# Optimization experiments

Hardware: AMD Instinct MI355X
Metric: run time of the kernel (lower is better)

Reference implementation:

```python
import jax, jax.numpy as jnp
import numpy as np

C = 1.0
SQC = C ** 0.5
EPS = 1e-15

def _artanh(x):
    return jnp.arctanh(jnp.clip(x, -1 + 1e-5, 1 - 1e-5))

def _norm(x):
    return jnp.sqrt(jnp.maximum(jnp.sum(x * x, -1, keepdims=True), EPS))

def expmap0(u):
    un = _norm(u)
    return jnp.tanh(SQC * un) * u / (SQC * un)

def logmap0(x):
    xn = _norm(x)
    return _artanh(SQC * xn) * x / (SQC * xn)

def project(x):
    maxnorm = (1.0 - 1e-3) / SQC
    xn = _norm(x)
    return jnp.where(xn > maxnorm, x / xn * maxnorm, x)

def mobius_add(x, y):
    x2 = jnp.sum(x * x, -1, keepdims=True)
    y2 = jnp.sum(y * y, -1, keepdims=True)
    xy = jnp.sum(x * y, -1, keepdims=True)
    num = (1 + 2 * C * xy + C * y2) * x + (1 - C * x2) * y
    den = 1 + 2 * C * xy + C * C * x2 * y2
    return num / jnp.maximum(den, EPS)

def mobius_matvec(M, x):
    xn = _norm(x)
    Mx = x @ M.T
    Mxn = _norm(Mx)
    res = jnp.tanh(Mxn / xn * _artanh(SQC * xn)) * Mx / (Mxn * SQC)
    return jnp.where(Mxn <= 1e-7, jnp.zeros_like(res), res)

def mobius_pointwise_mul(w, x):
    xn = _norm(x)
    wx = w * x
    wxn = _norm(wx)
    res = jnp.tanh(wxn / xn * _artanh(SQC * xn)) * wx / (wxn * SQC)
    return jnp.where(wxn <= 1e-7, jnp.zeros_like(res), res)

def mobius_scalar_mul(r, x):
    # r: [B,1] scalars, x: [P] point -> [B,P]
    xn = _norm(x)
    return jnp.tanh(r * _artanh(SQC * xn)) * x / (xn * SQC)

def poincare_dist(x, y):
    return 2.0 / SQC * _artanh(SQC * _norm(mobius_add(-x, y)))

def dist2plane(x, p, a):
    # x: [B,P], p,a: [K,P] -> [B,K]
    diff = mobius_add(-p[None, :, :], x[:, None, :])  # [B,K,P]
    diff2 = jnp.sum(diff * diff, -1)
    sc_da = jnp.sum(diff * a[None, :, :], -1)
    a_norm = jnp.sqrt(jnp.maximum(jnp.sum(a * a, -1), EPS))  # [K]
    num = 2 * SQC * sc_da
    den = jnp.maximum((1 - C * diff2) * a_norm[None, :], EPS)
    return jnp.arcsinh(num / den) / SQC

def one_rnn_transform(W, h, U, x, b):
    Wh = mobius_matvec(W, h)
    Ux = mobius_matvec(U, x)
    return mobius_add(mobius_add(Wh, Ux), b)

def mobius_gru(x_seq, w_ih, w_hh, b, h0):
    # x_seq: [S,B,E]; w_ih: [3,H,E]; w_hh: [3,H,H]; b: [3,H]
    W_ir, W_ih_, W_iz = w_ih[0], w_ih[1], w_ih[2]
    W_hr, W_hh_, W_hz = w_hh[0], w_hh[1], w_hh[2]
    b_r, b_h, b_z = b[0], b[1], b[2]

    def cell(h, x):
        z = jax.nn.sigmoid(logmap0(one_rnn_transform(W_hz, h, W_iz, x, b_z)))
        r = jax.nn.sigmoid(logmap0(one_rnn_transform(W_hr, h, W_ir, x, b_r)))
        rh = mobius_pointwise_mul(r, h)
        h_tilde = one_rnn_transform(W_hh_, rh, W_ih_, x, b_h)
        delta = mobius_add(-h, h_tilde)
        h_new = mobius_add(h, mobius_pointwise_mul(z, delta))
        return h_new, None

    h_final, _ = jax.lax.scan(cell, h0, x_seq)
    return h_final

def mobius_linear(x, W, b):
    return project(mobius_add(mobius_matvec(W, x), b))


def setup_inputs() -> dict:
    key = jax.random.key(0)
    ks = jax.random.split(key, 20)
    V, E, H, P, K, B, S = 32000, 256, 512, 256, 2, 512, 100
    inp = {
        "embedding": jax.random.normal(ks[0], (V, E), jnp.float32) * 0.1,
        "w_ih_src": jax.random.normal(ks[1], (3, H, E), jnp.float32) * 0.05,
        "w_hh_src": jax.random.normal(ks[2], (3, H, H), jnp.float32) * 0.05,
        "b_src": jax.random.normal(ks[3], (3, H), jnp.float32) * 0.01,
        "w_ih_tgt": jax.random.normal(ks[4], (3, H, E), jnp.float32) * 0.05,
        "w_hh_tgt": jax.random.normal(ks[5], (3, H, H), jnp.float32) * 0.05,
        "b_tgt": jax.random.normal(ks[6], (3, H), jnp.float32) * 0.01,
        "wp_src": jax.random.normal(ks[7], (P, H), jnp.float32) * 0.05,
        "bp_src": jax.random.normal(ks[8], (P,), jnp.float32) * 0.01,
        "wp_tgt": jax.random.normal(ks[9], (P, H), jnp.float32) * 0.05,
        "bp_tgt": jax.random.normal(ks[10], (P,), jnp.float32) * 0.01,
        "dist_bias": jax.random.normal(ks[11], (P,), jnp.float32) * 0.01,
        "plane_p": jax.random.normal(ks[12], (K, P), jnp.float32) * 0.01,
        "plane_a": jax.random.normal(ks[13], (K, P), jnp.float32) * 0.1,
        "source_tokens": jax.random.randint(ks[14], (B, S), 0, V, jnp.int32),
        "target_tokens": jax.random.randint(ks[15], (B, S), 0, V, jnp.int32),
        "alignment": jax.random.randint(ks[16], (B,), 0, B, jnp.int32),
    }
    return inp


def reference(embedding, w_ih_src, w_hh_src, b_src, w_ih_tgt, w_hh_tgt, b_tgt,
              wp_src, bp_src, wp_tgt, bp_tgt, dist_bias, plane_p, plane_a,
              source_tokens, target_tokens, alignment):
    B, S = source_tokens.shape
    H = w_hh_src.shape[-1]
    # euclidean embeddings lifted to the Poincare ball (embedding_type='eucl', hyp cell)
    src = expmap0(embedding[source_tokens]).transpose(1, 0, 2)  # [S,B,E]
    tgt = expmap0(embedding[target_tokens]).transpose(1, 0, 2)
    h0 = jnp.zeros((B, H), src.dtype)
    h_src = mobius_gru(src, w_ih_src, w_hh_src, b_src, h0)
    h_tgt = mobius_gru(tgt, w_ih_tgt, w_hh_tgt, b_tgt, h0)
    h_tgt = h_tgt[alignment]
    src_proj = mobius_linear(h_src, wp_src, bp_src)
    tgt_proj = mobius_linear(h_tgt, wp_tgt, bp_tgt)
    projected = mobius_add(src_proj, tgt_proj)
    d2 = poincare_dist(h_src, h_tgt) ** 2  # [B,1]
    bias = mobius_scalar_mul(d2, dist_bias)  # [B,P]
    projected = mobius_add(projected, bias)
    logits = dist2plane(projected, plane_p, plane_a)  # [B,K]
    return logits
```

## Files before the change

### kernel.cpp

```cpp
#include <hip/hip_runtime.h>
#include <hip/hip_bf16.h>

#define EPSF 1e-15f

__device__ __forceinline__ float artanh_c(float x) {
  x = fminf(fmaxf(x, -1.f + 1e-5f), 1.f - 1e-5f);
  return 0.5f * log1pf(2.f * x / (1.f - x));
}
__device__ __forceinline__ float sigmoidf(float x) {
  return 1.f / (1.f + expf(-x));
}

template<int N>
__device__ __forceinline__ void block_reduce(float* v) {
  __shared__ float s[4][N];
  __syncthreads();
  const int lane = threadIdx.x & 63;
  const int wv = threadIdx.x >> 6;
#pragma unroll
  for (int n = 0; n < N; n++) {
    float x = v[n];
#pragma unroll
    for (int o = 32; o > 0; o >>= 1) x += __shfl_down(x, o);
    if (lane == 0) s[wv][n] = x;
  }
  __syncthreads();
#pragma unroll
  for (int n = 0; n < N; n++) v[n] = s[0][n] + s[1][n] + s[2][n] + s[3][n];
}

__global__ __launch_bounds__(256) void k_tok(
    const float* __restrict__ emb, const int* __restrict__ src_t,
    const int* __restrict__ tgt_t, float4* __restrict__ tokf)
{
  const int item = blockIdx.x * 4 + (threadIdx.x >> 6);
  const int lane = threadIdx.x & 63;
  const int g = item / 51200;
  const int rem = item - g * 51200;
  const int b = rem / 100, s = rem - b * 100;
  const int tok = (g ? tgt_t : src_t)[b * 100 + s];
  const float4 v = ((const float4*)(emb + (size_t)tok * 256))[lane];
  float ss = v.x*v.x + v.y*v.y + v.z*v.z + v.w*v.w;
#pragma unroll
  for (int o = 32; o > 0; o >>= 1) ss += __shfl_xor(ss, o);
  if (lane == 0) {
    const float un = sqrtf(fmaxf(ss, EPSF));
    const float fac = tanhf(un) / un;
    const float xn = sqrtf(fmaxf(fac * fac * ss, EPSF));
    const float axn = artanh_c(xn);
    tokf[item] = make_float4(fac, xn, axn, un);
  }
}

__global__ __launch_bounds__(256) void kx0(
    const float* __restrict__ emb, const int* __restrict__ src_t,
    const int* __restrict__ tgt_t, const float4* __restrict__ tokf,
    float* __restrict__ xb)
{
  const int row = blockIdx.x;
  const int t = threadIdx.x;
  const int g = row >> 9, b = row & 511;
  const int tok = (g ? tgt_t : src_t)[b * 100];
  const float fac = tokf[(g * 512 + b) * 100].x;
  xb[(size_t)row * 256 + t] = fac * emb[(size_t)tok * 256 + t];
}

__global__ __launch_bounds__(256) void gemm_k(
    int mode,
    const float* __restrict__ hbuf, const float* __restrict__ xbuf,
    const float* __restrict__ rhbuf,
    const float* __restrict__ w_ih_src, const float* __restrict__ w_hh_src,
    const float* __restrict__ w_ih_tgt, const float* __restrict__ w_hh_tgt,
    const float* __restrict__ wp_src, const float* __restrict__ wp_tgt,
    const int* __restrict__ alignment,
    float* __restrict__ out)
{
  const int rt = blockIdx.x, ct = blockIdx.y;
  const int rowBase = rt * 64;
  const int tid = threadIdx.x;
  int kdim, ldo, colBase;
  const float* W;
  const float* Abase;
  int gather = 0;
  if (mode == 0) {
    const int chunk = ct >> 3;
    colBase = ct * 64; ldo = 2560;
    const int g = rowBase >> 9;
    const float* wih = g ? w_ih_tgt : w_ih_src;
    const float* whh = g ? w_hh_tgt : w_hh_src;
    if (chunk == 0)      { W = whh + 2 * 512 * 512; Abase = hbuf; kdim = 512; }
    else if (chunk == 1) { W = whh;                 Abase = hbuf; kdim = 512; }
    else {
      kdim = 256; Abase = xbuf;
      W = (chunk == 2) ? (wih + 2 * 512 * 256) : ((chunk == 3) ? wih : (wih + 512 * 256));
    }
    W += (size_t)((ct & 7) * 64) * kdim;
  } else if (mode == 1) {
    const int g = rowBase >> 9;
    W = (g ? w_hh_tgt : w_hh_src) + 512 * 512 + (size_t)(ct * 64) * 512;
    Abase = rhbuf; kdim = 512; ldo = 512; colBase = ct * 64;
  } else {
    const int chunk = ct >> 2;
    colBase = ct * 64; ldo = 512; kdim = 512;
    W = (chunk ? wp_tgt : wp_src) + (size_t)((ct & 3) * 64) * 512;
    Abase = hbuf;
    gather = chunk;
  }
  const int ar = tid >> 2, ak = (tid & 3) * 4;
  int arow = rowBase + ar;
  if (mode == 2 && gather) arow = 512 + alignment[arow];
  const float* Arow = Abase + (size_t)arow * kdim;
  const float* Wrow = W + (size_t)(tid >> 2) * kdim + (tid & 3) * 4;

  __shared__ __align__(16) float As[16][68];
  __shared__ __align__(16) float Bs[16][68];
  float acc[4][4] = {{0.f}};
  const int ty = tid >> 4, tx = tid & 15;

  for (int k0 = 0; k0 < kdim; k0 += 16) {
    const float4 av = *(const float4*)(Arow + k0 + ak);
    const float4 bv = *(const float4*)(Wrow + k0);
    const int bj = tid >> 2;
    As[ak + 0][ar] = av.x; As[ak + 1][ar] = av.y; As[ak + 2][ar] = av.z; As[ak + 3][ar] = av.w;
    Bs[ak + 0][bj] = bv.x; Bs[ak + 1][bj] = bv.y; Bs[ak + 2][bj] = bv.z; Bs[ak + 3][bj] = bv.w;
    __syncthreads();
#pragma unroll
    for (int kk = 0; kk < 16; kk++) {
      const float4 a4 = *(const float4*)(&As[kk][ty * 4]);
      const float4 b4 = *(const float4*)(&Bs[kk][tx * 4]);
      acc[0][0] += a4.x * b4.x; acc[0][1] += a4.x * b4.y; acc[0][2] += a4.x * b4.z; acc[0][3] += a4.x * b4.w;
      acc[1][0] += a4.y * b4.x; acc[1][1] += a4.y * b4.y; acc[1][2] += a4.y * b4.z; acc[1][3] += a4.y * b4.w;
      acc[2][0] += a4.z * b4.x; acc[2][1] += a4.z * b4.y; acc[2][2] += a4.z * b4.z; acc[2][3] += a4.z * b4.w;
      acc[3][0] += a4.w * b4.x; acc[3][1] += a4.w * b4.y; acc[3][2] += a4.w * b4.z; acc[3][3] += a4.w * b4.w;
    }
    __syncthreads();
  }
#pragma unroll
  for (int r = 0; r < 4; r++) {
    float4 o; o.x = acc[r][0]; o.y = acc[r][1]; o.z = acc[r][2]; o.w = acc[r][3];
    *(float4*)(out + (size_t)(rowBase + ty * 4 + r) * ldo + colBase + tx * 4) = o;
  }
}

__global__ __launch_bounds__(256) void k2_gates(
    const float* __restrict__ g1, const float* __restrict__ hb,
    const float* __restrict__ b_src, const float* __restrict__ b_tgt,
    const float4* __restrict__ tokf,
    float* __restrict__ zb, float* __restrict__ rhb,
    float* __restrict__ uhxb, float* __restrict__ rn, int s)
{
  const int row = blockIdx.x;
  const int g = row >> 9, b = row & 511;
  const int t = threadIdx.x;
  const float* bb = g ? b_tgt : b_src;
  const float4 tf = tokf[(g * 512 + b) * 100 + s];
  const float xn_x = tf.y, axn_x = tf.z;
  const float* grow = g1 + (size_t)row * 2560;
  const float* hrow = hb + (size_t)row * 512;

  float h[2], whz[2], whr[2], uxz[2], uxr[2], uxh[2], bz[2], br[2];
  float r6[6] = {0, 0, 0, 0, 0, 0};
#pragma unroll
  for (int e = 0; e < 2; e++) {
    const int j = t + e * 256;
    h[e] = hrow[j];
    whz[e] = grow[j];        whr[e] = grow[512 + j];
    uxz[e] = grow[1024 + j]; uxr[e] = grow[1536 + j];
    uxh[e] = grow[2048 + j];
    bz[e] = bb[1024 + j];    br[e] = bb[j];
    r6[0] += h[e] * h[e];     r6[1] += whz[e] * whz[e]; r6[2] += whr[e] * whr[e];
    r6[3] += uxz[e] * uxz[e]; r6[4] += uxr[e] * uxr[e]; r6[5] += uxh[e] * uxh[e];
  }
  block_reduce<6>(r6);
  const float sh2 = r6[0];
  const float xn_h = sqrtf(fmaxf(sh2, EPSF)), axn_h = artanh_c(xn_h);

  const float mz = sqrtf(fmaxf(r6[1], EPSF)); const float tz = tanhf(mz / xn_h * axn_h);
  const float sz = (mz <= 1e-7f) ? 0.f : tz / mz; const float x2z = (mz <= 1e-7f) ? 0.f : tz * tz;
  const float mr = sqrtf(fmaxf(r6[2], EPSF)); const float tr = tanhf(mr / xn_h * axn_h);
  const float sr = (mr <= 1e-7f) ? 0.f : tr / mr; const float x2r = (mr <= 1e-7f) ? 0.f : tr * tr;
  const float muz = sqrtf(fmaxf(r6[3], EPSF)); const float tuz = tanhf(muz / xn_x * axn_x);
  const float suz = (muz <= 1e-7f) ? 0.f : tuz / muz; const float y2z = (muz <= 1e-7f) ? 0.f : tuz * tuz;
  const float mur = sqrtf(fmaxf(r6[4], EPSF)); const float tur = tanhf(mur / xn_x * axn_x);
  const float sur = (mur <= 1e-7f) ? 0.f : tur / mur; const float y2r = (mur <= 1e-7f) ? 0.f : tur * tur;
  const float muh = sqrtf(fmaxf(r6[5], EPSF)); const float tuh = tanhf(muh / xn_x * axn_x);
  const float suh = (muh <= 1e-7f) ? 0.f : tuh / muh; const float y2u = (muh <= 1e-7f) ? 0.f : tuh * tuh;

  float Wz[2], Uz[2], Wr[2], Ur[2];
  float dd[2] = {0, 0};
#pragma unroll
  for (int e = 0; e < 2; e++) {
    Wz[e] = sz * whz[e]; Uz[e] = suz * uxz[e];
    Wr[e] = sr * whr[e]; Ur[e] = sur * uxr[e];
    dd[0] += Wz[e] * Uz[e]; dd[1] += Wr[e] * Ur[e];
  }
  block_reduce<2>(dd);
  float t1z[2], t1r[2];
  {
    const float xy = dd[0];
    const float iv = 1.f / fmaxf(1.f + 2.f * xy + x2z * y2z, EPSF);
    const float c1 = 1.f + 2.f * xy + y2z, c2 = 1.f - x2z;
#pragma unroll
    for (int e = 0; e < 2; e++) t1z[e] = (c1 * Wz[e] + c2 * Uz[e]) * iv;
  }
  {
    const float xy = dd[1];
    const float iv = 1.f / fmaxf(1.f + 2.f * xy + x2r * y2r, EPSF);
    const float c1 = 1.f + 2.f * xy + y2r, c2 = 1.f - x2r;
#pragma unroll
    for (int e = 0; e < 2; e++) t1r[e] = (c1 * Wr[e] + c2 * Ur[e]) * iv;
  }
  float r6b[6] = {0, 0, 0, 0, 0, 0};
#pragma unroll
  for (int e = 0; e < 2; e++) {
    r6b[0] += t1z[e] * t1z[e]; r6b[1] += t1z[e] * bz[e]; r6b[2] += bz[e] * bz[e];
    r6b[3] += t1r[e] * t1r[e]; r6b[4] += t1r[e] * br[e]; r6b[5] += br[e] * br[e];
  }
  block_reduce<6>(r6b);
  float t2z[2], t2r[2];
  {
    const float x2 = r6b[0], xy = r6b[1], y2 = r6b[2];
    const float iv = 1.f / fmaxf(1.f + 2.f * xy + x2 * y2, EPSF);
    const float c1 = 1.f + 2.f * xy + y2, c2 = 1.f - x2;
#pragma unroll
    for (int e = 0; e < 2; e++) t2z[e] = (c1 * t1z[e] + c2 * bz[e]) * iv;
  }
  {
    const float x2 = r6b[3], xy = r6b[4], y2 = r6b[5];
    const float iv = 1.f / fmaxf(1.f + 2.f * xy + x2 * y2, EPSF);
    const float c1 = 1.f + 2.f * xy + y2, c2 = 1.f - x2;
#pragma unroll
    for (int e = 0; e < 2; e++) t2r[e] = (c1 * t1r[e] + c2 * br[e]) * iv;
  }
  float nn[2] = {0, 0};
#pragma unroll
  for (int e = 0; e < 2; e++) { nn[0] += t2z[e] * t2z[e]; nn[1] += t2r[e] * t2r[e]; }
  block_reduce<2>(nn);
  const float nz = sqrtf(fmaxf(nn[0], EPSF)); const float fz = artanh_c(nz) / nz;
  const float nr = sqrtf(fmaxf(nn[1], EPSF)); const float fr = artanh_c(nr) / nr;
  float zz[2], wx[2];
  float rw[1] = {0};
#pragma unroll
  for (int e = 0; e < 2; e++) {
    zz[e] = sigmoidf(fz * t2z[e]);
    const float rr = sigmoidf(fr * t2r[e]);
    wx[e] = rr * h[e];
    rw[0] += wx[e] * wx[e];
  }
  block_reduce<1>(rw);
  const float wxn = sqrtf(fmaxf(rw[0], EPSF));
  const float trh = tanhf(wxn / xn_h * axn_h);
  const float srh = (wxn <= 1e-7f) ? 0.f : trh / wxn;
  const float xn_rh = (wxn <= 1e-7f) ? sqrtf(EPSF) : fmaxf(trh, sqrtf(EPSF));
  const float axn_rh = artanh_c(xn_rh);
#pragma unroll
  for (int e = 0; e < 2; e++) {
    const int j = t + e * 256;
    zb[(size_t)row * 512 + j] = zz[e];
    rhb[(size_t)row * 512 + j] = srh * wx[e];
    uhxb[(size_t)row * 512 + j] = suh * uxh[e];
  }
  if (t == 0) {
    float* r8 = rn + row * 8;
    r8[0] = xn_h; r8[1] = axn_h; r8[2] = xn_rh; r8[3] = axn_rh; r8[4] = y2u; r8[5] = sh2;
  }
}

__global__ __launch_bounds__(256) void k4_update(
    const float* __restrict__ htm, const float* __restrict__ uhxb,
    const float* __restrict__ zb, float* __restrict__ hb,
    const float* __restrict__ b_src, const float* __restrict__ b_tgt,
    const float* __restrict__ rn, const float4* __restrict__ tokf,
    const int* __restrict__ src_t, const int* __restrict__ tgt_t,
    const float* __restrict__ emb, float* __restrict__ xb, int s)
{
  const int row = blockIdx.x;
  const int g = row >> 9, b = row & 511;
  const int t = threadIdx.x;
  const float* bb = g ? b_tgt : b_src;
  const float* r8 = rn + row * 8;
  const float xn_rh = r8[2], axn_rh = r8[3], y2u = r8[4], sh2 = r8[5];

  float mt_[2], ux[2], z[2], h[2], bh[2];
  float rA[2] = {0, 0};
#pragma unroll
  for (int e = 0; e < 2; e++) {
    const int j = t + e * 256;
    mt_[e] = htm[(size_t)row * 512 + j];
    ux[e] = uhxb[(size_t)row * 512 + j];
    z[e] = zb[(size_t)row * 512 + j];
    h[e] = hb[(size_t)row * 512 + j];
    bh[e] = bb[512 + j];
    rA[0] += mt_[e] * mt_[e];
    rA[1] += mt_[e] * ux[e];
  }
  block_reduce<2>(rA);
  const float m = sqrtf(fmaxf(rA[0], EPSF));
  const float tt = tanhf(m / xn_rh * axn_rh);
  const float st = (m <= 1e-7f) ? 0.f : tt / m;
  const float x2 = (m <= 1e-7f) ? 0.f : tt * tt;
  float t1[2];
  {
    const float xy = st * rA[1];
    const float iv = 1.f / fmaxf(1.f + 2.f * xy + x2 * y2u, EPSF);
    const float c1 = 1.f + 2.f * xy + y2u, c2 = 1.f - x2;
#pragma unroll
    for (int e = 0; e < 2; e++) t1[e] = (c1 * (st * mt_[e]) + c2 * ux[e]) * iv;
  }
  float rB[3] = {0, 0, 0};
#pragma unroll
  for (int e = 0; e < 2; e++) {
    rB[0] += t1[e] * t1[e]; rB[1] += t1[e] * bh[e]; rB[2] += bh[e] * bh[e];
  }
  block_reduce<3>(rB);
  float ht[2];
  {
    const float x2b = rB[0], xy = rB[1], y2 = rB[2];
    const float iv = 1.f / fmaxf(1.f + 2.f * xy + x2b * y2, EPSF);
    const float c1 = 1.f + 2.f * xy + y2, c2 = 1.f - x2b;
#pragma unroll
    for (int e = 0; e < 2; e++) ht[e] = (c1 * t1[e] + c2 * bh[e]) * iv;
  }
  float rC[2] = {0, 0};
#pragma unroll
  for (int e = 0; e < 2; e++) { rC[0] += ht[e] * ht[e]; rC[1] += h[e] * ht[e]; }
  block_reduce<2>(rC);
  float delta[2];
  {
    const float y2 = rC[0], xy = -rC[1];
    const float iv = 1.f / fmaxf(1.f + 2.f * xy + sh2 * y2, EPSF);
    const float c1 = 1.f + 2.f * xy + y2, c2 = 1.f - sh2;
#pragma unroll
    for (int e = 0; e < 2; e++) delta[e] = (c1 * (-h[e]) + c2 * ht[e]) * iv;
  }
  float rD[3] = {0, 0, 0};
#pragma unroll
  for (int e = 0; e < 2; e++) {
    const float w = z[e] * delta[e];
    rD[0] += delta[e] * delta[e];
    rD[1] += w * w;
    rD[2] += h[e] * w;
  }
  block_reduce<3>(rD);
  const float dn = sqrtf(fmaxf(rD[0], EPSF));
  const float axnd = artanh_c(dn);
  const float wxn = sqrtf(fmaxf(rD[1], EPSF));
  const float tzd = tanhf(wxn / dn * axnd);
  const float szd = (wxn <= 1e-7f) ? 0.f : tzd / wxn;
  const float y2zd = (wxn <= 1e-7f) ? 0.f : tzd * tzd;
  {
    const float xy = szd * rD[2];
    const float iv = 1.f / fmaxf(1.f + 2.f * xy + sh2 * y2zd, EPSF);
    const float c1 = 1.f + 2.f * xy + y2zd, c2 = 1.f - sh2;
#pragma unroll
    for (int e = 0; e < 2; e++) {
      const int j = t + e * 256;
      hb[(size_t)row * 512 + j] = (c1 * h[e] + c2 * (szd * z[e] * delta[e])) * iv;
    }
  }
  if (s + 1 < 100) {
    const int tok = (g ? tgt_t : src_t)[b * 100 + s + 1];
    const float fac = tokf[(g * 512 + b) * 100 + s + 1].x;
    xb[(size_t)row * 256 + t] = fac * emb[(size_t)tok * 256 + t];
  }
}

__global__ __launch_bounds__(256) void k_head(
    const float* __restrict__ hb, const float* __restrict__ mxb,
    const float* __restrict__ bp_src, const float* __restrict__ bp_tgt,
    const float* __restrict__ dist_bias, const float* __restrict__ plane_p,
    const float* __restrict__ plane_a, const int* __restrict__ alignment,
    float* __restrict__ outp)
{
  const int b = blockIdx.x;
  const int t = threadIdx.x;
  const int arow = 512 + alignment[b];
  float hs[2], htg[2];
  hs[0] = hb[(size_t)b * 512 + t];      hs[1] = hb[(size_t)b * 512 + 256 + t];
  htg[0] = hb[(size_t)arow * 512 + t];  htg[1] = hb[(size_t)arow * 512 + 256 + t];
  const float mxs = mxb[(size_t)b * 512 + t];
  const float mxt = mxb[(size_t)b * 512 + 256 + t];
  const float bps = bp_src[t], bpt = bp_tgt[t], db = dist_bias[t];
  const float pp0 = plane_p[t], pp1 = plane_p[256 + t];
  const float pa0 = plane_a[t], pa1 = plane_a[256 + t];

  float rA[5] = {0, 0, 0, 0, 0};
#pragma unroll
  for (int e = 0; e < 2; e++) {
    rA[0] += hs[e] * hs[e]; rA[1] += htg[e] * htg[e]; rA[2] += hs[e] * htg[e];
  }
  rA[3] = mxs * mxs; rA[4] = mxt * mxt;
  block_reduce<5>(rA);
  const float shs = rA[0], sht = rA[1], dot_st = rA[2];
  const float xns = sqrtf(fmaxf(shs, EPSF)), axns = artanh_c(xns);
  const float xnt = sqrtf(fmaxf(sht, EPSF)), axnt = artanh_c(xnt);
  const float ms = sqrtf(fmaxf(rA[3], EPSF)); const float ts = tanhf(ms / xns * axns);
  const float ss = (ms <= 1e-7f) ? 0.f : ts / ms; const float x2s = (ms <= 1e-7f) ? 0.f : ts * ts;
  const float mt = sqrtf(fmaxf(rA[4], EPSF)); const float tt = tanhf(mt / xnt * axnt);
  const float st = (mt <= 1e-7f) ? 0.f : tt / mt; const float x2t = (mt <= 1e-7f) ? 0.f : tt * tt;
  const float vs = ss * mxs, vt = st * mxt;

  float rB[5] = {bps * bps, vs * bps, bpt * bpt, vt * bpt, db * db};
  block_reduce<5>(rB);
  float ps, pt;
  {
    const float y2 = rB[0], xy = rB[1];
    const float iv = 1.f / fmaxf(1.f + 2.f * xy + x2s * y2, EPSF);
    ps = ((1.f + 2.f * xy + y2) * vs + (1.f - x2s) * bps) * iv;
  }
  {
    const float y2 = rB[2], xy = rB[3];
    const float iv = 1.f / fmaxf(1.f + 2.f * xy + x2t * y2, EPSF);
    pt = ((1.f + 2.f * xy + y2) * vt + (1.f - x2t) * bpt) * iv;
  }
  float rC[2] = {ps * ps, pt * pt};
  block_reduce<2>(rC);
  {
    const float n = sqrtf(fmaxf(rC[0], EPSF));
    if (n > 0.999f) ps *= 0.999f / n;
  }
  {
    const float n = sqrtf(fmaxf(rC[1], EPSF));
    if (n > 0.999f) pt *= 0.999f / n;
  }
  float df[2];
  {
    const float xy = -dot_st;
    const float iv = 1.f / fmaxf(1.f + 2.f * xy + shs * sht, EPSF);
    const float c1 = 1.f + 2.f * xy + sht, c2 = 1.f - shs;
#pragma unroll
    for (int e = 0; e < 2; e++) df[e] = (c1 * (-hs[e]) + c2 * htg[e]) * iv;
  }
  float rD[4] = {ps * ps, pt * pt, ps * pt, df[0] * df[0] + df[1] * df[1]};
  block_reduce<4>(rD);
  float pr;
  {
    const float x2 = rD[0], y2 = rD[1], xy = rD[2];
    const float iv = 1.f / fmaxf(1.f + 2.f * xy + x2 * y2, EPSF);
    pr = ((1.f + 2.f * xy + y2) * ps + (1.f - x2) * pt) * iv;
  }
  const float dn = sqrtf(fmaxf(rD[3], EPSF));
  const float dist = 2.f * artanh_c(dn);
  const float d2v = dist * dist;
  const float dbn = sqrtf(fmaxf(rB[4], EPSF));
  const float biasv = tanhf(d2v * artanh_c(dbn)) * db / dbn;

  float rE[3] = {pr * pr, biasv * biasv, pr * biasv};
  block_reduce<3>(rE);
  float pr2;
  {
    const float x2 = rE[0], y2 = rE[1], xy = rE[2];
    const float iv = 1.f / fmaxf(1.f + 2.f * xy + x2 * y2, EPSF);
    pr2 = ((1.f + 2.f * xy + y2) * pr + (1.f - x2) * biasv) * iv;
  }
  float rF[5] = {pp0 * pp0, pp0 * pr2, pp1 * pp1, pp1 * pr2, pr2 * pr2};
  block_reduce<5>(rF);
  float d0, d1;
  {
    const float x2 = rF[0], xy = -rF[1], y2 = rF[4];
    const float iv = 1.f / fmaxf(1.f + 2.f * xy + x2 * y2, EPSF);
    d0 = ((1.f + 2.f * xy + y2) * (-pp0) + (1.f - x2) * pr2) * iv;
  }
  {
    const float x2 = rF[2], xy = -rF[3], y2 = rF[4];
    const float iv = 1.f / fmaxf(1.f + 2.f * xy + x2 * y2, EPSF);
    d1 = ((1.f + 2.f * xy + y2) * (-pp1) + (1.f - x2) * pr2) * iv;
  }
  float rG[6] = {d0 * d0, d0 * pa0, pa0 * pa0, d1 * d1, d1 * pa1, pa1 * pa1};
  block_reduce<6>(rG);
  if (t == 0) {
    const float an0 = sqrtf(fmaxf(rG[2], EPSF));
    const float an1 = sqrtf(fmaxf(rG[5], EPSF));
    const float l0 = asinhf(2.f * rG[1] / fmaxf((1.f - rG[0]) * an0, EPSF));
    const float l1 = asinhf(2.f * rG[4] / fmaxf((1.f - rG[3]) * an1, EPSF));
    outp[b * 2 + 0] = l0;
    outp[b * 2 + 1] = l1;
  }
}

extern "C" void kernel_launch(void* const* d_in, const int* in_sizes, int n_in,
                              void* d_out, int out_size, void* d_ws, size_t ws_size,
                              hipStream_t stream) {
  const float* emb       = (const float*)d_in[0];
  const float* w_ih_src  = (const float*)d_in[1];
  const float* w_hh_src  = (const float*)d_in[2];
  const float* b_src     = (const float*)d_in[3];
  const float* w_ih_tgt  = (const float*)d_in[4];
  const float* w_hh_tgt  = (const float*)d_in[5];
  const float* b_tgt     = (const float*)d_in[6];
  const float* wp_src    = (const float*)d_in[7];
  const float* bp_src    = (const float*)d_in[8];
  const float* wp_tgt    = (const float*)d_in[9];
  const float* bp_tgt    = (const float*)d_in[10];
  const float* dist_bias = (const float*)d_in[11];
  const float* plane_p   = (const float*)d_in[12];
  const float* plane_a   = (const float*)d_in[13];
  const int* src_t       = (const int*)d_in[14];
  const int* tgt_t       = (const int*)d_in[15];
  const int* alignment   = (const int*)d_in[16];
  float* outp            = (float*)d_out;

  float* ws = (float*)d_ws;
  float* hbuf = ws + 0;
  float* xbuf = ws + 524288;
  float* g1   = ws + 786432;
  float* zb   = ws + 3407872;
  float* rhb  = ws + 3932160;
  float* uhxb = ws + 4456448;
  float* htm  = ws + 4980736;
  float* rn   = ws + 5505024;
  float4* tokf = (float4*)(ws + 5513216);
  float* mxb  = ws + 5922816;

  hipMemsetAsync(hbuf, 0, 1024 * 512 * sizeof(float), stream);
  k_tok<<<25600, 256, 0, stream>>>(emb, src_t, tgt_t, tokf);
  kx0<<<1024, 256, 0, stream>>>(emb, src_t, tgt_t, tokf, xbuf);
  for (int s = 0; s < 100; s++) {
    gemm_k<<<dim3(16, 40), 256, 0, stream>>>(0, hbuf, xbuf, rhb,
        w_ih_src, w_hh_src, w_ih_tgt, w_hh_tgt, wp_src, wp_tgt, alignment, g1);
    k2_gates<<<1024, 256, 0, stream>>>(g1, hbuf, b_src, b_tgt, tokf, zb, rhb, uhxb, rn, s);
    gemm_k<<<dim3(16, 8), 256, 0, stream>>>(1, hbuf, xbuf, rhb,
        w_ih_src, w_hh_src, w_ih_tgt, w_hh_tgt, wp_src, wp_tgt, alignment, htm);
    k4_update<<<1024, 256, 0, stream>>>(htm, uhxb, zb, hbuf, b_src, b_tgt, rn, tokf,
        src_t, tgt_t, emb, xbuf, s);
  }
  gemm_k<<<dim3(8, 8), 256, 0, stream>>>(2, hbuf, xbuf, rhb,
      w_ih_src, w_hh_src, w_ih_tgt, w_hh_tgt, wp_src, wp_tgt, alignment, mxb);
  k_head<<<512, 256, 0, stream>>>(hbuf, mxb, bp_src, bp_tgt, dist_bias,
      plane_p, plane_a, alignment, outp);
}
```

Before: 8.037 ms.

## Use split-bf16 MFMA GEMMs for GRU recurrent and input projections

The per-step fp32 SIMT GEMMs are replaced with an MFMA kernel that emulates fp32 accuracy by splitting each operand into high and low bf16 parts and summing three bf16 products. Weights are converted once up front. The hidden state, input and reset-gated state are written in split bf16 form by the producer kernels. This moves the dominant matmul work onto matrix cores, at the cost of extra conversion stores, doubled operand loads without LDS staging, and a small loss of precision from dropping the low-by-low term.

```diff
diff --git a/kernel.cpp b/kernel.cpp
--- a/kernel.cpp
+++ b/kernel.cpp
@@ -2,6 +2,10 @@
 #include <hip/hip_bf16.h>
 
 #define EPSF 1e-15f
+
+typedef __hip_bfloat16 bf16;
+typedef __attribute__((ext_vector_type(8))) short short8;
+typedef __attribute__((ext_vector_type(4))) float f32x4;
 
 __device__ __forceinline__ float artanh_c(float x) {
   x = fminf(fmaxf(x, -1.f + 1e-5f), 1.f - 1e-5f);
@@ -9,6 +13,12 @@
 }
 __device__ __forceinline__ float sigmoidf(float x) {
   return 1.f / (1.f + expf(-x));
+}
+__device__ __forceinline__ void split_store(float v, bf16* __restrict__ ph,
+                                            bf16* __restrict__ pl, size_t i) {
+  const bf16 hi = __float2bfloat16(v);
+  ph[i] = hi;
+  pl[i] = __float2bfloat16(v - __bfloat162float(hi));
 }
 
 template<int N>
@@ -27,6 +37,35 @@
   __syncthreads();
 #pragma unroll
   for (int n = 0; n < N; n++) v[n] = s[0][n] + s[1][n] + s[2][n] + s[3][n];
+}
+
+__global__ __launch_bounds__(256) void k_wconv(
+    const float* __restrict__ w_ih_src, const float* __restrict__ w_hh_src,
+    const float* __restrict__ w_ih_tgt, const float* __restrict__ w_hh_tgt,
+    bf16* __restrict__ W0h, bf16* __restrict__ W0l,
+    bf16* __restrict__ W1h, bf16* __restrict__ W1l)
+{
+  const int idx = blockIdx.x * 256 + threadIdx.x;
+  float v; bf16 *ph, *pl; int oi;
+  if (idx < 1835008) {
+    const int g = idx / 917504, r = idx % 917504;
+    const float* wih = g ? w_ih_tgt : w_ih_src;
+    const float* whh = g ? w_hh_tgt : w_hh_src;
+    if (r < 262144)      v = whh[524288 + r];
+    else if (r < 524288) v = whh[r - 262144];
+    else if (r < 655360) v = wih[262144 + (r - 524288)];
+    else if (r < 786432) v = wih[r - 655360];
+    else                 v = wih[131072 + (r - 786432)];
+    ph = W0h; pl = W0l; oi = idx;
+  } else {
+    const int j = idx - 1835008;
+    if (j >= 524288) return;
+    const int g = j >> 18, r = j & 262143;
+    const float* whh = g ? w_hh_tgt : w_hh_src;
+    v = whh[262144 + r];
+    ph = W1h; pl = W1l; oi = j;
+  }
+  split_store(v, ph, pl, oi);
 }
 
 __global__ __launch_bounds__(256) void k_tok(
@@ -55,14 +94,91 @@
 __global__ __launch_bounds__(256) void kx0(
     const float* __restrict__ emb, const int* __restrict__ src_t,
     const int* __restrict__ tgt_t, const float4* __restrict__ tokf,
-    float* __restrict__ xb)
+    bf16* __restrict__ Xh, bf16* __restrict__ Xl)
 {
   const int row = blockIdx.x;
   const int t = threadIdx.x;
   const int g = row >> 9, b = row & 511;
   const int tok = (g ? tgt_t : src_t)[b * 100];
   const float fac = tokf[(g * 512 + b) * 100].x;
-  xb[(size_t)row * 256 + t] = fac * emb[(size_t)tok * 256 + t];
+  split_store(fac * emb[(size_t)tok * 256 + t], Xh, Xl, (size_t)row * 256 + t);
+}
+
+__global__ __launch_bounds__(512) void gemm_mfma(
+    int mode,
+    const bf16* __restrict__ Hh, const bf16* __restrict__ Hl,
+    const bf16* __restrict__ Xh, const bf16* __restrict__ Xl,
+    const bf16* __restrict__ Rh, const bf16* __restrict__ Rl,
+    const bf16* __restrict__ W0h, const bf16* __restrict__ W0l,
+    const bf16* __restrict__ W1h, const bf16* __restrict__ W1l,
+    float* __restrict__ out)
+{
+  const int rt = blockIdx.x, ct = blockIdx.y;
+  const int rowBase = rt * 128;
+  const int tid = threadIdx.x;
+  const int w = tid >> 6, lane = tid & 63;
+  const int wr = w >> 1, wc = w & 1;
+  const int fr = lane & 15, kg = lane >> 4;
+
+  int K, ldo, colBase;
+  const bf16 *Ah, *Al, *Wh, *Wl;
+  if (mode == 0) {
+    const int chunk = ct >> 3;
+    colBase = ct * 64; ldo = 2560;
+    const int g = rowBase >> 9;
+    int chOff;
+    if (chunk < 2) { Ah = Hh; Al = Hl; K = 512; chOff = chunk * 262144; }
+    else           { Ah = Xh; Al = Xl; K = 256; chOff = 524288 + (chunk - 2) * 131072; }
+    const size_t wb = (size_t)g * 917504 + chOff + (size_t)((ct & 7) * 64) * K;
+    Wh = W0h + wb; Wl = W0l + wb;
+  } else {
+    colBase = ct * 64; ldo = 512; K = 512;
+    const int g = rowBase >> 9;
+    const size_t wb = (size_t)g * 262144 + (size_t)(ct * 64) * 512;
+    Wh = W1h + wb; Wl = W1l + wb;
+    Ah = Rh; Al = Rl;
+  }
+  const int r0 = rowBase + wr * 32;
+  const int lc = wc * 32 + fr;
+  const size_t a0off = (size_t)(r0 + fr) * K + kg * 8;
+  const size_t a1off = a0off + (size_t)16 * K;
+  const size_t b0off = (size_t)lc * K + kg * 8;
+  const size_t b1off = b0off + (size_t)16 * K;
+
+  f32x4 acc00 = {0.f,0.f,0.f,0.f}, acc01 = {0.f,0.f,0.f,0.f};
+  f32x4 acc10 = {0.f,0.f,0.f,0.f}, acc11 = {0.f,0.f,0.f,0.f};
+
+#pragma unroll 2
+  for (int k0 = 0; k0 < K; k0 += 32) {
+    const short8 a0h = *(const short8*)(Ah + a0off + k0);
+    const short8 a0l = *(const short8*)(Al + a0off + k0);
+    const short8 a1h = *(const short8*)(Ah + a1off + k0);
+    const short8 a1l = *(const short8*)(Al + a1off + k0);
+    const short8 b0h = *(const short8*)(Wh + b0off + k0);
+    const short8 b0l = *(const short8*)(Wl + b0off + k0);
+    const short8 b1h = *(const short8*)(Wh + b1off + k0);
+    const short8 b1l = *(const short8*)(Wl + b1off + k0);
+    acc00 = __builtin_amdgcn_mfma_f32_16x16x32_bf16(a0h, b0h, acc00, 0, 0, 0);
+    acc01 = __builtin_amdgcn_mfma_f32_16x16x32_bf16(a0h, b1h, acc01, 0, 0, 0);
+    acc10 = __builtin_amdgcn_mfma_f32_16x16x32_bf16(a1h, b0h, acc10, 0, 0, 0);
+    acc11 = __builtin_amdgcn_mfma_f32_16x16x32_bf16(a1h, b1h, acc11, 0, 0, 0);
+    acc00 = __builtin_amdgcn_mfma_f32_16x16x32_bf16(a0h, b0l, acc00, 0, 0, 0);
+    acc01 = __builtin_amdgcn_mfma_f32_16x16x32_bf16(a0h, b1l, acc01, 0, 0, 0);
+    acc10 = __builtin_amdgcn_mfma_f32_16x16x32_bf16(a1h, b0l, acc10, 0, 0, 0);
+    acc11 = __builtin_amdgcn_mfma_f32_16x16x32_bf16(a1h, b1l, acc11, 0, 0, 0);
+    acc00 = __builtin_amdgcn_mfma_f32_16x16x32_bf16(a0l, b0h, acc00, 0, 0, 0);
+    acc01 = __builtin_amdgcn_mfma_f32_16x16x32_bf16(a0l, b1h, acc01, 0, 0, 0);
+    acc10 = __builtin_amdgcn_mfma_f32_16x16x32_bf16(a1l, b0h, acc10, 0, 0, 0);
+    acc11 = __builtin_amdgcn_mfma_f32_16x16x32_bf16(a1l, b1h, acc11, 0, 0, 0);
+  }
+  const int cb = colBase + wc * 32 + fr;
+#pragma unroll
+  for (int r = 0; r < 4; r++) {
+    out[(size_t)(r0 + kg*4 + r) * ldo + cb]           = acc00[r];
+    out[(size_t)(r0 + kg*4 + r) * ldo + cb + 16]      = acc01[r];
+    out[(size_t)(r0 + 16 + kg*4 + r) * ldo + cb]      = acc10[r];
+    out[(size_t)(r0 + 16 + kg*4 + r) * ldo + cb + 16] = acc11[r];
+  }
 }
 
 __global__ __launch_bounds__(256) void gemm_k(
@@ -82,24 +198,7 @@
   const float* W;
   const float* Abase;
   int gather = 0;
-  if (mode == 0) {
-    const int chunk = ct >> 3;
-    colBase = ct * 64; ldo = 2560;
-    const int g = rowBase >> 9;
-    const float* wih = g ? w_ih_tgt : w_ih_src;
-    const float* whh = g ? w_hh_tgt : w_hh_src;
-    if (chunk == 0)      { W = whh + 2 * 512 * 512; Abase = hbuf; kdim = 512; }
-    else if (chunk == 1) { W = whh;                 Abase = hbuf; kdim = 512; }
-    else {
-      kdim = 256; Abase = xbuf;
-      W = (chunk == 2) ? (wih + 2 * 512 * 256) : ((chunk == 3) ? wih : (wih + 512 * 256));
-    }
-    W += (size_t)((ct & 7) * 64) * kdim;
-  } else if (mode == 1) {
-    const int g = rowBase >> 9;
-    W = (g ? w_hh_tgt : w_hh_src) + 512 * 512 + (size_t)(ct * 64) * 512;
-    Abase = rhbuf; kdim = 512; ldo = 512; colBase = ct * 64;
-  } else {
+  {
     const int chunk = ct >> 2;
     colBase = ct * 64; ldo = 512; kdim = 512;
     W = (chunk ? wp_tgt : wp_src) + (size_t)((ct & 3) * 64) * 512;
@@ -108,7 +207,7 @@
   }
   const int ar = tid >> 2, ak = (tid & 3) * 4;
   int arow = rowBase + ar;
-  if (mode == 2 && gather) arow = 512 + alignment[arow];
+  if (gather) arow = 512 + alignment[arow];
   const float* Arow = Abase + (size_t)arow * kdim;
   const float* Wrow = W + (size_t)(tid >> 2) * kdim + (tid & 3) * 4;
 
@@ -146,7 +245,7 @@
     const float* __restrict__ g1, const float* __restrict__ hb,
     const float* __restrict__ b_src, const float* __restrict__ b_tgt,
     const float4* __restrict__ tokf,
-    float* __restrict__ zb, float* __restrict__ rhb,
+    float* __restrict__ zb, bf16* __restrict__ Rh, bf16* __restrict__ Rl,
     float* __restrict__ uhxb, float* __restrict__ rn, int s)
 {
   const int row = blockIdx.x;
@@ -257,7 +356,7 @@
   for (int e = 0; e < 2; e++) {
     const int j = t + e * 256;
     zb[(size_t)row * 512 + j] = zz[e];
-    rhb[(size_t)row * 512 + j] = srh * wx[e];
+    split_store(srh * wx[e], Rh, Rl, (size_t)row * 512 + j);
     uhxb[(size_t)row * 512 + j] = suh * uxh[e];
   }
   if (t == 0) {
@@ -272,7 +371,9 @@
     const float* __restrict__ b_src, const float* __restrict__ b_tgt,
     const float* __restrict__ rn, const float4* __restrict__ tokf,
     const int* __restrict__ src_t, const int* __restrict__ tgt_t,
-    const float* __restrict__ emb, float* __restrict__ xb, int s)
+    const float* __restrict__ emb,
+    bf16* __restrict__ Hh, bf16* __restrict__ Hl,
+    bf16* __restrict__ Xh, bf16* __restrict__ Xl, int s)
 {
   const int row = blockIdx.x;
   const int g = row >> 9, b = row & 511;
@@ -355,13 +456,15 @@
 #pragma unroll
     for (int e = 0; e < 2; e++) {
       const int j = t + e * 256;
-      hb[(size_t)row * 512 + j] = (c1 * h[e] + c2 * (szd * z[e] * delta[e])) * iv;
+      const float hn = (c1 * h[e] + c2 * (szd * z[e] * delta[e])) * iv;
+      hb[(size_t)row * 512 + j] = hn;
+      split_store(hn, Hh, Hl, (size_t)row * 512 + j);
     }
   }
   if (s + 1 < 100) {
     const int tok = (g ? tgt_t : src_t)[b * 100 + s + 1];
     const float fac = tokf[(g * 512 + b) * 100 + s + 1].x;
-    xb[(size_t)row * 256 + t] = fac * emb[(size_t)tok * 256 + t];
+    split_store(fac * emb[(size_t)tok * 256 + t], Xh, Xl, (size_t)row * 256 + t);
   }
 }
 
@@ -500,31 +603,43 @@
   const int* alignment   = (const int*)d_in[16];
   float* outp            = (float*)d_out;
 
-  float* ws = (float*)d_ws;
-  float* hbuf = ws + 0;
-  float* xbuf = ws + 524288;
-  float* g1   = ws + 786432;
-  float* zb   = ws + 3407872;
-  float* rhb  = ws + 3932160;
-  float* uhxb = ws + 4456448;
-  float* htm  = ws + 4980736;
-  float* rn   = ws + 5505024;
-  float4* tokf = (float4*)(ws + 5513216);
-  float* mxb  = ws + 5922816;
-
-  hipMemsetAsync(hbuf, 0, 1024 * 512 * sizeof(float), stream);
+  char* wsb = (char*)d_ws;
+  float*  hbuf = (float*)(wsb + 0);
+  float*  g1   = (float*)(wsb + 2097152);
+  float*  zb   = (float*)(wsb + 12582912);
+  float*  uhxb = (float*)(wsb + 14680064);
+  float*  htm  = (float*)(wsb + 16777216);
+  float*  rn   = (float*)(wsb + 18874368);
+  float4* tokf = (float4*)(wsb + 18907136);
+  float*  mxb  = (float*)(wsb + 20545536);
+  bf16*   Hh   = (bf16*)(wsb + 21594112);
+  bf16*   Hl   = (bf16*)(wsb + 22642688);
+  bf16*   Xh   = (bf16*)(wsb + 23691264);
+  bf16*   Xl   = (bf16*)(wsb + 24215552);
+  bf16*   Rh   = (bf16*)(wsb + 24739840);
+  bf16*   Rl   = (bf16*)(wsb + 25788416);
+  bf16*   W0h  = (bf16*)(wsb + 26836992);
+  bf16*   W0l  = (bf16*)(wsb + 30507008);
+  bf16*   W1h  = (bf16*)(wsb + 34177024);
+  bf16*   W1l  = (bf16*)(wsb + 35225600);
+
+  hipMemsetAsync(hbuf, 0, 2097152, stream);
+  hipMemsetAsync(Hh, 0, 1048576, stream);
+  hipMemsetAsync(Hl, 0, 1048576, stream);
+  k_wconv<<<9216, 256, 0, stream>>>(w_ih_src, w_hh_src, w_ih_tgt, w_hh_tgt,
+                                    W0h, W0l, W1h, W1l);
   k_tok<<<25600, 256, 0, stream>>>(emb, src_t, tgt_t, tokf);
-  kx0<<<1024, 256, 0, stream>>>(emb, src_t, tgt_t, tokf, xbuf);
+  kx0<<<1024, 256, 0, stream>>>(emb, src_t, tgt_t, tokf, Xh, Xl);
   for (int s = 0; s < 100; s++) {
-    gemm_k<<<dim3(16, 40), 256, 0, stream>>>(0, hbuf, xbuf, rhb,
-        w_ih_src, w_hh_src, w_ih_tgt, w_hh_tgt, wp_src, wp_tgt, alignment, g1);
-    k2_gates<<<1024, 256, 0, stream>>>(g1, hbuf, b_src, b_tgt, tokf, zb, rhb, uhxb, rn, s);
-    gemm_k<<<dim3(16, 8), 256, 0, stream>>>(1, hbuf, xbuf, rhb,
-        w_ih_src, w_hh_src, w_ih_tgt, w_hh_tgt, wp_src, wp_tgt, alignment, htm);
+    gemm_mfma<<<dim3(8, 40), 512, 0, stream>>>(0, Hh, Hl, Xh, Xl, Rh, Rl,
+        W0h, W0l, W1h, W1l, g1);
+    k2_gates<<<1024, 256, 0, stream>>>(g1, hbuf, b_src, b_tgt, tokf, zb, Rh, Rl, uhxb, rn, s);
+    gemm_mfma<<<dim3(8, 8), 512, 0, stream>>>(1, Hh, Hl, Xh, Xl, Rh, Rl,
+        W0h, W0l, W1h, W1l, htm);
     k4_update<<<1024, 256, 0, stream>>>(htm, uhxb, zb, hbuf, b_src, b_tgt, rn, tokf,
-        src_t, tgt_t, emb, xbuf, s);
-  }
-  gemm_k<<<dim3(8, 8), 256, 0, stream>>>(2, hbuf, xbuf, rhb,
+        src_t, tgt_t, emb, Hh, Hl, Xh, Xl, s);
+  }
+  gemm_k<<<dim3(8, 8), 256, 0, stream>>>(2, hbuf, hbuf, hbuf,
       w_ih_src, w_hh_src, w_ih_tgt, w_hh_tgt, wp_src, wp_tgt, alignment, mxb);
   k_head<<<512, 256, 0, stream>>>(hbuf, mxb, bp_src, bp_tgt, dist_bias,
       plane_p, plane_a, alignment, outp);
```

New measurement: 9.866 ms. +22.7%, slower.
